# Kernel optimization log

Hardware: AMD Instinct MI355X
Metric: run time of the kernel (lower is better)

The kernel has to match this reference:

```python
import jax, jax.numpy as jnp
import numpy as np

N, D_IN, R, D_OUT, U = 500000, 128, 256, 64, 10000
EPS = 1e-8


def _vb_layer(m, v, W_mu, W_lv, relu_out):
    # Variational Bayes linear layer, moment propagation:
    #   out_mean = m @ W_mu
    #   out_var  = v @ (W_mu^2 + W_var) + m^2 @ W_var,  W_var = exp(W_lv)
    W_var = jnp.exp(W_lv)
    M = m @ W_mu
    V = v @ (W_mu * W_mu + W_var) + (m * m) @ W_var
    if relu_out:
        gate = (M > 0).astype(M.dtype)
        M = M * gate
        V = V * gate
    return M, V


def setup_inputs() -> dict:
    key = jax.random.key(0)
    ks = jax.random.split(key, 6)
    X = jax.random.normal(ks[0], (N, D_IN), jnp.float32)
    X_idx = jnp.sort(jax.random.randint(ks[1], (N,), 0, U, dtype=jnp.int32))
    W_mu0 = jax.random.normal(ks[2], (D_IN, R), jnp.float32) / np.sqrt(D_IN)
    W_lv0 = jax.random.normal(ks[3], (D_IN, R), jnp.float32) * 0.1 - 4.0
    W_mu1 = jax.random.normal(ks[4], (R, D_OUT), jnp.float32) / np.sqrt(R)
    W_lv1 = jax.random.normal(ks[5], (R, D_OUT), jnp.float32) * 0.1 - 4.0
    return {"X": X, "X_idx": X_idx, "W_mu0": W_mu0, "W_lv0": W_lv0,
            "W_mu1": W_mu1, "W_lv1": W_lv1}


def reference(X, X_idx, W_mu0, W_lv0, W_mu1, W_lv1):
    m, v = _vb_layer(X, jnp.zeros_like(X), W_mu0, W_lv0, True)   # [N, R]
    m, v = _vb_layer(m, v, W_mu1, W_lv1, False)                  # [N, D_OUT]
    v = jnp.maximum(v, EPS)
    inv_v = 1.0 / v
    # precision-weighted aggregation per group id (replaces per-uid loop)
    var_inv_sum = jax.ops.segment_sum(inv_v, X_idx, num_segments=U) + EPS
    mean_sum = jax.ops.segment_sum(m * inv_v, X_idx, num_segments=U)
    emb_var = 1.0 / var_inv_sum          # [U, D_OUT]
    emb_mean = mean_sum * emb_var        # [U, D_OUT]
    return emb_mean, emb_var
```

## Files before the change

kernel.cpp:

```cpp
#include <hip/hip_runtime.h>
#include <stdint.h>

#define N_ROWS 500000
#define U_DIM 10000
#define EPSV 1e-8f
#define NT16 31250

typedef __attribute__((ext_vector_type(8))) short bf16x8;
typedef __attribute__((ext_vector_type(4))) float f32x4;

__device__ __forceinline__ short f2bf(float f) {
  unsigned u = __float_as_uint(f);
  u += 0x7fffu + ((u >> 16) & 1u);
  return (short)(u >> 16);
}
__device__ __forceinline__ float bf2f(short s) {
  return __uint_as_float(((unsigned)(unsigned short)s) << 16);
}

__global__ void prep_weights(const float* __restrict__ Wmu0,
                             const float* __restrict__ Wlv0,
                             const float* __restrict__ Wmu1,
                             const float* __restrict__ Wlv1,
                             short* __restrict__ wgt) {
  int i = blockIdx.x * blockDim.x + threadIdx.x;
  if (i < 32768) {
    int c = i & 255, k = i >> 8;
    int rc = c >> 5, ct = (c >> 4) & 1, n = c & 15;
    int kt = k >> 5, q = (k >> 3) & 3, u = k & 7;
    int lane = q * 16 + n;
    float mu = Wmu0[k * 256 + c];
    float ev = __expf(Wlv0[k * 256 + c]);
    wgt[((((rc * 2 + 0) * 2 + ct) * 4 + kt) * 64 + lane) * 8 + u] = f2bf(mu);
    wgt[((((rc * 2 + 1) * 2 + ct) * 4 + kt) * 64 + lane) * 8 + u] = f2bf(ev);
  } else if (i < 49152) {
    int i2 = i - 32768;
    int o = i2 & 63, j = i2 >> 6;
    int rc = j >> 5, q = (j >> 3) & 3, u = j & 7;
    int ct1 = o >> 4, n = o & 15;
    int lane = q * 16 + n;
    float mu = Wmu1[j * 64 + o];
    float ev = __expf(Wlv1[j * 64 + o]);
    int b = 65536 + (((rc * 4 + ct1) * 3 + 0) * 64 + lane) * 8 + u;
    wgt[b]        = f2bf(mu);
    wgt[b + 512]  = f2bf(mu * mu + ev);
    wgt[b + 1024] = f2bf(ev);
  }
}

__global__ __launch_bounds__(256, 3) void vb_fused(
    const float* __restrict__ X, const int* __restrict__ Xidx,
    const short* __restrict__ wgt, float* __restrict__ out) {
  __shared__ __align__(16) short stage[2][8192];
  __shared__ __align__(16) short ldsM[4][16 * 40];
  __shared__ __align__(16) short ldsV[4][16 * 40];

  const int tid  = threadIdx.x;
  const int w    = tid >> 6;
  const int lane = tid & 63;
  const int n    = lane & 15;
  const int q    = lane >> 4;
  const int T    = blockIdx.x * 4 + w;
  const bool active = (T < NT16);
  const int row0 = active ? T * 16 : (N_ROWS - 16);

  const f32x4 zf4 = {0.f, 0.f, 0.f, 0.f};
  const int lane8 = lane * 8;

  bf16x8 a_m[4], a_sq[4];
  {
    const float* xr = X + (size_t)(row0 + n) * 128;
#pragma unroll
    for (int kt = 0; kt < 4; ++kt) {
      float xf[8];
      *(float4*)&xf[0] = *(const float4*)&xr[kt * 32 + q * 8];
      *(float4*)&xf[4] = *(const float4*)&xr[kt * 32 + q * 8 + 4];
#pragma unroll
      for (int u = 0; u < 8; ++u) {
        a_m[kt][u]  = f2bf(xf[u]);
        a_sq[kt][u] = f2bf(xf[u] * xf[u]);
      }
    }
  }

  f32x4 accm1[4], accv1[4];
#pragma unroll
  for (int c = 0; c < 4; ++c) { accm1[c] = zf4; accv1[c] = zf4; }

  const char* gbase = (const char*)wgt;
#define ISSUE_STAGE(rc_, buf_)                                                 \
  do {                                                                         \
    _Pragma("unroll")                                                          \
    for (int s_ = 0; s_ < 4; ++s_) {                                           \
      __builtin_amdgcn_global_load_lds(                                        \
          (const __attribute__((address_space(1))) unsigned int*)              \
              (gbase + (rc_) * 16384 + s_ * 4096 + tid * 16),                  \
          (__attribute__((address_space(3))) unsigned int*)                    \
              ((char*)&stage[buf_][0] + s_ * 4096 + (w << 10)),                \
          16, 0, 0);                                                           \
    }                                                                          \
  } while (0)

  ISSUE_STAGE(0, 0);

#pragma unroll
  for (int rc = 0; rc < 8; ++rc) {
    __syncthreads();
    if (rc < 7) ISSUE_STAGE(rc + 1, (rc + 1) & 1);

    const short* st = &stage[rc & 1][0];

    f32x4 accm0[2], accv0[2];
    accm0[0] = zf4; accm0[1] = zf4; accv0[0] = zf4; accv0[1] = zf4;
#pragma unroll
    for (int kt = 0; kt < 4; ++kt) {
#pragma unroll
      for (int ct = 0; ct < 2; ++ct) {
        bf16x8 bm = *(const bf16x8*)&st[((0 * 2 + ct) * 4 + kt) * 512 + lane8];
        bf16x8 bv = *(const bf16x8*)&st[((1 * 2 + ct) * 4 + kt) * 512 + lane8];
        accm0[ct] = __builtin_amdgcn_mfma_f32_16x16x32_bf16(a_m[kt],  bm, accm0[ct], 0, 0, 0);
        accv0[ct] = __builtin_amdgcn_mfma_f32_16x16x32_bf16(a_sq[kt], bv, accv0[ct], 0, 0, 0);
      }
    }

#pragma unroll
    for (int ct = 0; ct < 2; ++ct) {
      const int c = ct * 16 + n;
#pragma unroll
      for (int reg = 0; reg < 4; ++reg) {
        float m = accm0[ct][reg], v = accv0[ct][reg];
        if (!(m > 0.f)) { m = 0.f; v = 0.f; }
        const int row = q * 4 + reg;
        ldsM[w][row * 40 + c] = f2bf(m);
        ldsV[w][row * 40 + c] = f2bf(v);
      }
    }
    bf16x8 am = *(const bf16x8*)&ldsM[w][n * 40 + q * 8];
    bf16x8 av = *(const bf16x8*)&ldsV[w][n * 40 + q * 8];
    bf16x8 asq;
#pragma unroll
    for (int u = 0; u < 8; ++u) {
      float f = bf2f(am[u]);
      asq[u] = f2bf(f * f);
    }

    const short* l1b = wgt + 65536 + rc * 6144 + lane8;
#pragma unroll
    for (int ct1 = 0; ct1 < 4; ++ct1) {
      const short* fb = l1b + ct1 * 1536;
      bf16x8 b1 = *(const bf16x8*)&fb[0];
      bf16x8 b2 = *(const bf16x8*)&fb[512];
      bf16x8 b3 = *(const bf16x8*)&fb[1024];
      accm1[ct1] = __builtin_amdgcn_mfma_f32_16x16x32_bf16(am,  b1, accm1[ct1], 0, 0, 0);
      accv1[ct1] = __builtin_amdgcn_mfma_f32_16x16x32_bf16(av,  b2, accv1[ct1], 0, 0, 0);
      accv1[ct1] = __builtin_amdgcn_mfma_f32_16x16x32_bf16(asq, b3, accv1[ct1], 0, 0, 0);
    }
  }
#undef ISSUE_STAGE

  if (!active) return;
  float* meanp = out;
  float* varp  = out + U_DIM * 64;
  int4 idx4 = *(const int4*)&Xidx[row0 + q * 4];
  int uid[4] = {idx4.x, idx4.y, idx4.z, idx4.w};
#pragma unroll
  for (int ct = 0; ct < 4; ++ct) {
    const int o = ct * 16 + n;
    float sm = 0.f, sv = 0.f;
    int cur = uid[0];
#pragma unroll
    for (int reg = 0; reg < 4; ++reg) {
      float v1 = fmaxf(accv1[ct][reg], EPSV);
      float inv = 1.0f / v1;
      float mi  = accm1[ct][reg] * inv;
      if (uid[reg] != cur) {
        atomicAdd(&meanp[cur * 64 + o], sm);
        atomicAdd(&varp[cur * 64 + o], sv);
        sm = 0.f; sv = 0.f; cur = uid[reg];
      }
      sm += mi; sv += inv;
    }
    atomicAdd(&meanp[cur * 64 + o], sm);
    atomicAdd(&varp[cur * 64 + o], sv);
  }
}

__global__ void finalize(float* __restrict__ out) {
  int i = blockIdx.x * blockDim.x + threadIdx.x;
  if (i < U_DIM * 64) {
    float s = out[U_DIM * 64 + i];
    float var = 1.0f / (s + EPSV);
    out[U_DIM * 64 + i] = var;
    out[i] = out[i] * var;
  }
}

extern "C" void kernel_launch(void* const* d_in, const int* in_sizes, int n_in,
                              void* d_out, int out_size, void* d_ws, size_t ws_size,
                              hipStream_t stream) {
  (void)in_sizes; (void)n_in; (void)out_size; (void)ws_size;
  const float* X    = (const float*)d_in[0];
  const int*   Xidx = (const int*)d_in[1];
  const float* Wmu0 = (const float*)d_in[2];
  const float* Wlv0 = (const float*)d_in[3];
  const float* Wmu1 = (const float*)d_in[4];
  const float* Wlv1 = (const float*)d_in[5];
  float* out = (float*)d_out;
  short* wgt = (short*)d_ws;

  hipMemsetAsync(d_out, 0, (size_t)U_DIM * 64 * 2 * sizeof(float), stream);
  prep_weights<<<192, 256, 0, stream>>>(Wmu0, Wlv0, Wmu1, Wlv1, wgt);
  vb_fused<<<7813, 256, 0, stream>>>(X, Xidx, wgt, out);
  finalize<<<(U_DIM * 64 + 255) / 256, 256, 0, stream>>>(out);
}
```

Measured before the change: 555.9 us.

## Make fused VB kernel persistent with full layer-0 weights resident in LDS

Switches from one-tile-per-wave blocks to a persistent grid of 256 blocks of 8 waves. Each block loads all 128 KB of layer-0 weights into LDS once, then loops over 16-row tiles with a stride of 2048. Each wave prefetches the next tile's X rows into registers while computing the current one. This removes the per-block restaging of weights and the per-stage barriers, at the cost of lower occupancy from the large LDS footprint. With 256 blocks on 256 CUs there is only one block per CU.

```diff
diff --git a/kernel.cpp b/kernel.cpp
--- a/kernel.cpp
+++ b/kernel.cpp
@@ -48,140 +48,158 @@
   }
 }
 
-__global__ __launch_bounds__(256, 3) void vb_fused(
+__global__ __launch_bounds__(512, 2) void vb_fused(
     const float* __restrict__ X, const int* __restrict__ Xidx,
     const short* __restrict__ wgt, float* __restrict__ out) {
-  __shared__ __align__(16) short stage[2][8192];
-  __shared__ __align__(16) short ldsM[4][16 * 40];
-  __shared__ __align__(16) short ldsV[4][16 * 40];
+  __shared__ __align__(16) short stage[65536];
+  __shared__ __align__(16) short ldsM[8][16 * 40];
+  __shared__ __align__(16) short ldsV[8][16 * 40];
 
   const int tid  = threadIdx.x;
   const int w    = tid >> 6;
   const int lane = tid & 63;
   const int n    = lane & 15;
   const int q    = lane >> 4;
-  const int T    = blockIdx.x * 4 + w;
-  const bool active = (T < NT16);
-  const int row0 = active ? T * 16 : (N_ROWS - 16);
-
+  const int lane8 = lane * 8;
+
+  {
+    const char* gbase = (const char*)wgt;
+#pragma unroll
+    for (int s = 0; s < 16; ++s) {
+      __builtin_amdgcn_global_load_lds(
+          (const __attribute__((address_space(1))) unsigned int*)
+              (gbase + s * 8192 + tid * 16),
+          (__attribute__((address_space(3))) unsigned int*)
+              ((char*)&stage[0] + s * 8192 + (w << 10)),
+          16, 0, 0);
+    }
+  }
+  __syncthreads();
+
+  const int gw = blockIdx.x * 8 + w;
+  int T = gw;
+
+  float* meanp = out;
+  float* varp  = out + U_DIM * 64;
   const f32x4 zf4 = {0.f, 0.f, 0.f, 0.f};
-  const int lane8 = lane * 8;
-
-  bf16x8 a_m[4], a_sq[4];
+
+  float4 xr[8];
   {
-    const float* xr = X + (size_t)(row0 + n) * 128;
+    const float* xp = X + (size_t)(T * 16 + n) * 128 + q * 8;
+#pragma unroll
+    for (int kt = 0; kt < 4; ++kt) {
+      xr[kt * 2]     = *(const float4*)(xp + kt * 32);
+      xr[kt * 2 + 1] = *(const float4*)(xp + kt * 32 + 4);
+    }
+  }
+
+  while (true) {
+    bf16x8 a_m[4], a_sq[4];
 #pragma unroll
     for (int kt = 0; kt < 4; ++kt) {
       float xf[8];
-      *(float4*)&xf[0] = *(const float4*)&xr[kt * 32 + q * 8];
-      *(float4*)&xf[4] = *(const float4*)&xr[kt * 32 + q * 8 + 4];
+      *(float4*)&xf[0] = xr[kt * 2];
+      *(float4*)&xf[4] = xr[kt * 2 + 1];
 #pragma unroll
       for (int u = 0; u < 8; ++u) {
         a_m[kt][u]  = f2bf(xf[u]);
         a_sq[kt][u] = f2bf(xf[u] * xf[u]);
       }
     }
-  }
-
-  f32x4 accm1[4], accv1[4];
-#pragma unroll
-  for (int c = 0; c < 4; ++c) { accm1[c] = zf4; accv1[c] = zf4; }
-
-  const char* gbase = (const char*)wgt;
-#define ISSUE_STAGE(rc_, buf_)                                                 \
-  do {                                                                         \
-    _Pragma("unroll")                                                          \
-    for (int s_ = 0; s_ < 4; ++s_) {                                           \
-      __builtin_amdgcn_global_load_lds(                                        \
-          (const __attribute__((address_space(1))) unsigned int*)              \
-              (gbase + (rc_) * 16384 + s_ * 4096 + tid * 16),                  \
-          (__attribute__((address_space(3))) unsigned int*)                    \
-              ((char*)&stage[buf_][0] + s_ * 4096 + (w << 10)),                \
-          16, 0, 0);                                                           \
-    }                                                                          \
-  } while (0)
-
-  ISSUE_STAGE(0, 0);
-
-#pragma unroll
-  for (int rc = 0; rc < 8; ++rc) {
-    __syncthreads();
-    if (rc < 7) ISSUE_STAGE(rc + 1, (rc + 1) & 1);
-
-    const short* st = &stage[rc & 1][0];
-
-    f32x4 accm0[2], accv0[2];
-    accm0[0] = zf4; accm0[1] = zf4; accv0[0] = zf4; accv0[1] = zf4;
-#pragma unroll
-    for (int kt = 0; kt < 4; ++kt) {
+
+    const int Tcur = T;
+    const int Tn   = T + 2048;
+    if (Tn < NT16) {
+      const float* xp = X + (size_t)(Tn * 16 + n) * 128 + q * 8;
+#pragma unroll
+      for (int kt = 0; kt < 4; ++kt) {
+        xr[kt * 2]     = *(const float4*)(xp + kt * 32);
+        xr[kt * 2 + 1] = *(const float4*)(xp + kt * 32 + 4);
+      }
+    }
+
+    f32x4 accm1[4], accv1[4];
+#pragma unroll
+    for (int c = 0; c < 4; ++c) { accm1[c] = zf4; accv1[c] = zf4; }
+
+#pragma unroll
+    for (int rc = 0; rc < 8; ++rc) {
+      const short* st = &stage[rc * 8192];
+
+      f32x4 accm0[2], accv0[2];
+      accm0[0] = zf4; accm0[1] = zf4; accv0[0] = zf4; accv0[1] = zf4;
+#pragma unroll
+      for (int kt = 0; kt < 4; ++kt) {
+#pragma unroll
+        for (int ct = 0; ct < 2; ++ct) {
+          bf16x8 bm = *(const bf16x8*)&st[((0 * 2 + ct) * 4 + kt) * 512 + lane8];
+          bf16x8 bv = *(const bf16x8*)&st[((1 * 2 + ct) * 4 + kt) * 512 + lane8];
+          accm0[ct] = __builtin_amdgcn_mfma_f32_16x16x32_bf16(a_m[kt],  bm, accm0[ct], 0, 0, 0);
+          accv0[ct] = __builtin_amdgcn_mfma_f32_16x16x32_bf16(a_sq[kt], bv, accv0[ct], 0, 0, 0);
+        }
+      }
+
 #pragma unroll
       for (int ct = 0; ct < 2; ++ct) {
-        bf16x8 bm = *(const bf16x8*)&st[((0 * 2 + ct) * 4 + kt) * 512 + lane8];
-        bf16x8 bv = *(const bf16x8*)&st[((1 * 2 + ct) * 4 + kt) * 512 + lane8];
-        accm0[ct] = __builtin_amdgcn_mfma_f32_16x16x32_bf16(a_m[kt],  bm, accm0[ct], 0, 0, 0);
-        accv0[ct] = __builtin_amdgcn_mfma_f32_16x16x32_bf16(a_sq[kt], bv, accv0[ct], 0, 0, 0);
-      }
-    }
-
-#pragma unroll
-    for (int ct = 0; ct < 2; ++ct) {
-      const int c = ct * 16 + n;
-#pragma unroll
-      for (int reg = 0; reg < 4; ++reg) {
-        float m = accm0[ct][reg], v = accv0[ct][reg];
-        if (!(m > 0.f)) { m = 0.f; v = 0.f; }
-        const int row = q * 4 + reg;
-        ldsM[w][row * 40 + c] = f2bf(m);
-        ldsV[w][row * 40 + c] = f2bf(v);
-      }
-    }
-    bf16x8 am = *(const bf16x8*)&ldsM[w][n * 40 + q * 8];
-    bf16x8 av = *(const bf16x8*)&ldsV[w][n * 40 + q * 8];
-    bf16x8 asq;
-#pragma unroll
-    for (int u = 0; u < 8; ++u) {
-      float f = bf2f(am[u]);
-      asq[u] = f2bf(f * f);
-    }
-
-    const short* l1b = wgt + 65536 + rc * 6144 + lane8;
-#pragma unroll
-    for (int ct1 = 0; ct1 < 4; ++ct1) {
-      const short* fb = l1b + ct1 * 1536;
-      bf16x8 b1 = *(const bf16x8*)&fb[0];
-      bf16x8 b2 = *(const bf16x8*)&fb[512];
-      bf16x8 b3 = *(const bf16x8*)&fb[1024];
-      accm1[ct1] = __builtin_amdgcn_mfma_f32_16x16x32_bf16(am,  b1, accm1[ct1], 0, 0, 0);
-      accv1[ct1] = __builtin_amdgcn_mfma_f32_16x16x32_bf16(av,  b2, accv1[ct1], 0, 0, 0);
-      accv1[ct1] = __builtin_amdgcn_mfma_f32_16x16x32_bf16(asq, b3, accv1[ct1], 0, 0, 0);
-    }
-  }
-#undef ISSUE_STAGE
-
-  if (!active) return;
-  float* meanp = out;
-  float* varp  = out + U_DIM * 64;
-  int4 idx4 = *(const int4*)&Xidx[row0 + q * 4];
-  int uid[4] = {idx4.x, idx4.y, idx4.z, idx4.w};
-#pragma unroll
-  for (int ct = 0; ct < 4; ++ct) {
-    const int o = ct * 16 + n;
-    float sm = 0.f, sv = 0.f;
-    int cur = uid[0];
-#pragma unroll
-    for (int reg = 0; reg < 4; ++reg) {
-      float v1 = fmaxf(accv1[ct][reg], EPSV);
-      float inv = 1.0f / v1;
-      float mi  = accm1[ct][reg] * inv;
-      if (uid[reg] != cur) {
+        const int c = ct * 16 + n;
+#pragma unroll
+        for (int reg = 0; reg < 4; ++reg) {
+          float m = accm0[ct][reg], v = accv0[ct][reg];
+          if (!(m > 0.f)) { m = 0.f; v = 0.f; }
+          const int row = q * 4 + reg;
+          ldsM[w][row * 40 + c] = f2bf(m);
+          ldsV[w][row * 40 + c] = f2bf(v);
+        }
+      }
+      bf16x8 am = *(const bf16x8*)&ldsM[w][n * 40 + q * 8];
+      bf16x8 av = *(const bf16x8*)&ldsV[w][n * 40 + q * 8];
+      bf16x8 asq;
+#pragma unroll
+      for (int u = 0; u < 8; ++u) {
+        float f = bf2f(am[u]);
+        asq[u] = f2bf(f * f);
+      }
+
+      const short* l1b = wgt + 65536 + rc * 6144 + lane8;
+#pragma unroll
+      for (int ct1 = 0; ct1 < 4; ++ct1) {
+        const short* fb = l1b + ct1 * 1536;
+        bf16x8 b1 = *(const bf16x8*)&fb[0];
+        bf16x8 b2 = *(const bf16x8*)&fb[512];
+        bf16x8 b3 = *(const bf16x8*)&fb[1024];
+        accm1[ct1] = __builtin_amdgcn_mfma_f32_16x16x32_bf16(am,  b1, accm1[ct1], 0, 0, 0);
+        accv1[ct1] = __builtin_amdgcn_mfma_f32_16x16x32_bf16(av,  b2, accv1[ct1], 0, 0, 0);
+        accv1[ct1] = __builtin_amdgcn_mfma_f32_16x16x32_bf16(asq, b3, accv1[ct1], 0, 0, 0);
+      }
+    }
+
+    {
+      int4 idx4 = *(const int4*)&Xidx[Tcur * 16 + q * 4];
+      int uid[4] = {idx4.x, idx4.y, idx4.z, idx4.w};
+#pragma unroll
+      for (int ct = 0; ct < 4; ++ct) {
+        const int o = ct * 16 + n;
+        float sm = 0.f, sv = 0.f;
+        int cur = uid[0];
+#pragma unroll
+        for (int reg = 0; reg < 4; ++reg) {
+          float v1 = fmaxf(accv1[ct][reg], EPSV);
+          float inv = 1.0f / v1;
+          float mi  = accm1[ct][reg] * inv;
+          if (uid[reg] != cur) {
+            atomicAdd(&meanp[cur * 64 + o], sm);
+            atomicAdd(&varp[cur * 64 + o], sv);
+            sm = 0.f; sv = 0.f; cur = uid[reg];
+          }
+          sm += mi; sv += inv;
+        }
         atomicAdd(&meanp[cur * 64 + o], sm);
         atomicAdd(&varp[cur * 64 + o], sv);
-        sm = 0.f; sv = 0.f; cur = uid[reg];
-      }
-      sm += mi; sv += inv;
-    }
-    atomicAdd(&meanp[cur * 64 + o], sm);
-    atomicAdd(&varp[cur * 64 + o], sv);
+      }
+    }
+
+    if (Tn >= NT16) break;
+    T = Tn;
   }
 }
 
@@ -210,6 +228,6 @@
 
   hipMemsetAsync(d_out, 0, (size_t)U_DIM * 64 * 2 * sizeof(float), stream);
   prep_weights<<<192, 256, 0, stream>>>(Wmu0, Wlv0, Wmu1, Wlv1, wgt);
-  vb_fused<<<7813, 256, 0, stream>>>(X, Xidx, wgt, out);
+  vb_fused<<<256, 512, 0, stream>>>(X, Xidx, wgt, out);
   finalize<<<(U_DIM * 64 + 255) / 256, 256, 0, stream>>>(out);
 }
```

Result: slower. 870.7 us (+56.6%).

## Process two 16-row tiles per wave to reuse staged weights

Applied to the files above, without the earlier changes.

Each wave now handles 32 rows as two 16-row MFMA tiles, sharing every weight fragment loaded from LDS and global across both tiles. The grid is halved accordingly, and the LDS scratch for layer-0 activations is doubled. This cuts the weight staging, barrier and fragment-load overhead per row. The cost is higher register pressure under the existing launch bounds, with possible spills, and fewer blocks in flight.

```diff
diff --git a/kernel.cpp b/kernel.cpp
--- a/kernel.cpp
+++ b/kernel.cpp
@@ -4,7 +4,7 @@
 #define N_ROWS 500000
 #define U_DIM 10000
 #define EPSV 1e-8f
-#define NT16 31250
+#define NT32 15625
 
 typedef __attribute__((ext_vector_type(8))) short bf16x8;
 typedef __attribute__((ext_vector_type(4))) float f32x4;
@@ -52,8 +52,8 @@
     const float* __restrict__ X, const int* __restrict__ Xidx,
     const short* __restrict__ wgt, float* __restrict__ out) {
   __shared__ __align__(16) short stage[2][8192];
-  __shared__ __align__(16) short ldsM[4][16 * 40];
-  __shared__ __align__(16) short ldsV[4][16 * 40];
+  __shared__ __align__(16) short ldsM[4][2][16 * 40];
+  __shared__ __align__(16) short ldsV[4][2][16 * 40];
 
   const int tid  = threadIdx.x;
   const int w    = tid >> 6;
@@ -61,15 +61,16 @@
   const int n    = lane & 15;
   const int q    = lane >> 4;
   const int T    = blockIdx.x * 4 + w;
-  const bool active = (T < NT16);
-  const int row0 = active ? T * 16 : (N_ROWS - 16);
+  const bool active = (T < NT32);
+  const int row0 = active ? T * 32 : (N_ROWS - 32);
 
   const f32x4 zf4 = {0.f, 0.f, 0.f, 0.f};
   const int lane8 = lane * 8;
 
-  bf16x8 a_m[4], a_sq[4];
-  {
-    const float* xr = X + (size_t)(row0 + n) * 128;
+  bf16x8 a_m[2][4], a_sq[2][4];
+#pragma unroll
+  for (int t = 0; t < 2; ++t) {
+    const float* xr = X + (size_t)(row0 + t * 16 + n) * 128;
 #pragma unroll
     for (int kt = 0; kt < 4; ++kt) {
       float xf[8];
@@ -77,15 +78,17 @@
       *(float4*)&xf[4] = *(const float4*)&xr[kt * 32 + q * 8 + 4];
 #pragma unroll
       for (int u = 0; u < 8; ++u) {
-        a_m[kt][u]  = f2bf(xf[u]);
-        a_sq[kt][u] = f2bf(xf[u] * xf[u]);
-      }
-    }
-  }
-
-  f32x4 accm1[4], accv1[4];
-#pragma unroll
-  for (int c = 0; c < 4; ++c) { accm1[c] = zf4; accv1[c] = zf4; }
+        a_m[t][kt][u]  = f2bf(xf[u]);
+        a_sq[t][kt][u] = f2bf(xf[u] * xf[u]);
+      }
+    }
+  }
+
+  f32x4 accm1[2][4], accv1[2][4];
+#pragma unroll
+  for (int t = 0; t < 2; ++t)
+#pragma unroll
+    for (int c = 0; c < 4; ++c) { accm1[t][c] = zf4; accv1[t][c] = zf4; }
 
   const char* gbase = (const char*)wgt;
 #define ISSUE_STAGE(rc_, buf_)                                                 \
@@ -110,38 +113,43 @@
 
     const short* st = &stage[rc & 1][0];
 
-    f32x4 accm0[2], accv0[2];
-    accm0[0] = zf4; accm0[1] = zf4; accv0[0] = zf4; accv0[1] = zf4;
-#pragma unroll
-    for (int kt = 0; kt < 4; ++kt) {
-#pragma unroll
-      for (int ct = 0; ct < 2; ++ct) {
+#pragma unroll
+    for (int ct = 0; ct < 2; ++ct) {
+      f32x4 am0_0 = zf4, am0_1 = zf4, av0_0 = zf4, av0_1 = zf4;
+#pragma unroll
+      for (int kt = 0; kt < 4; ++kt) {
         bf16x8 bm = *(const bf16x8*)&st[((0 * 2 + ct) * 4 + kt) * 512 + lane8];
         bf16x8 bv = *(const bf16x8*)&st[((1 * 2 + ct) * 4 + kt) * 512 + lane8];
-        accm0[ct] = __builtin_amdgcn_mfma_f32_16x16x32_bf16(a_m[kt],  bm, accm0[ct], 0, 0, 0);
-        accv0[ct] = __builtin_amdgcn_mfma_f32_16x16x32_bf16(a_sq[kt], bv, accv0[ct], 0, 0, 0);
-      }
-    }
-
-#pragma unroll
-    for (int ct = 0; ct < 2; ++ct) {
+        am0_0 = __builtin_amdgcn_mfma_f32_16x16x32_bf16(a_m[0][kt],  bm, am0_0, 0, 0, 0);
+        am0_1 = __builtin_amdgcn_mfma_f32_16x16x32_bf16(a_m[1][kt],  bm, am0_1, 0, 0, 0);
+        av0_0 = __builtin_amdgcn_mfma_f32_16x16x32_bf16(a_sq[0][kt], bv, av0_0, 0, 0, 0);
+        av0_1 = __builtin_amdgcn_mfma_f32_16x16x32_bf16(a_sq[1][kt], bv, av0_1, 0, 0, 0);
+      }
       const int c = ct * 16 + n;
 #pragma unroll
       for (int reg = 0; reg < 4; ++reg) {
-        float m = accm0[ct][reg], v = accv0[ct][reg];
-        if (!(m > 0.f)) { m = 0.f; v = 0.f; }
         const int row = q * 4 + reg;
-        ldsM[w][row * 40 + c] = f2bf(m);
-        ldsV[w][row * 40 + c] = f2bf(v);
-      }
-    }
-    bf16x8 am = *(const bf16x8*)&ldsM[w][n * 40 + q * 8];
-    bf16x8 av = *(const bf16x8*)&ldsV[w][n * 40 + q * 8];
-    bf16x8 asq;
-#pragma unroll
-    for (int u = 0; u < 8; ++u) {
-      float f = bf2f(am[u]);
-      asq[u] = f2bf(f * f);
+        float m0 = am0_0[reg], v0 = av0_0[reg];
+        if (!(m0 > 0.f)) { m0 = 0.f; v0 = 0.f; }
+        ldsM[w][0][row * 40 + c] = f2bf(m0);
+        ldsV[w][0][row * 40 + c] = f2bf(v0);
+        float m1 = am0_1[reg], v1 = av0_1[reg];
+        if (!(m1 > 0.f)) { m1 = 0.f; v1 = 0.f; }
+        ldsM[w][1][row * 40 + c] = f2bf(m1);
+        ldsV[w][1][row * 40 + c] = f2bf(v1);
+      }
+    }
+
+    bf16x8 am[2], av[2], asq[2];
+#pragma unroll
+    for (int t = 0; t < 2; ++t) {
+      am[t] = *(const bf16x8*)&ldsM[w][t][n * 40 + q * 8];
+      av[t] = *(const bf16x8*)&ldsV[w][t][n * 40 + q * 8];
+#pragma unroll
+      for (int u = 0; u < 8; ++u) {
+        float f = bf2f(am[t][u]);
+        asq[t][u] = f2bf(f * f);
+      }
     }
 
     const short* l1b = wgt + 65536 + rc * 6144 + lane8;
@@ -151,9 +159,12 @@
       bf16x8 b1 = *(const bf16x8*)&fb[0];
       bf16x8 b2 = *(const bf16x8*)&fb[512];
       bf16x8 b3 = *(const bf16x8*)&fb[1024];
-      accm1[ct1] = __builtin_amdgcn_mfma_f32_16x16x32_bf16(am,  b1, accm1[ct1], 0, 0, 0);
-      accv1[ct1] = __builtin_amdgcn_mfma_f32_16x16x32_bf16(av,  b2, accv1[ct1], 0, 0, 0);
-      accv1[ct1] = __builtin_amdgcn_mfma_f32_16x16x32_bf16(asq, b3, accv1[ct1], 0, 0, 0);
+#pragma unroll
+      for (int t = 0; t < 2; ++t) {
+        accm1[t][ct1] = __builtin_amdgcn_mfma_f32_16x16x32_bf16(am[t],  b1, accm1[t][ct1], 0, 0, 0);
+        accv1[t][ct1] = __builtin_amdgcn_mfma_f32_16x16x32_bf16(av[t],  b2, accv1[t][ct1], 0, 0, 0);
+        accv1[t][ct1] = __builtin_amdgcn_mfma_f32_16x16x32_bf16(asq[t], b3, accv1[t][ct1], 0, 0, 0);
+      }
     }
   }
 #undef ISSUE_STAGE
@@ -161,27 +172,30 @@
   if (!active) return;
   float* meanp = out;
   float* varp  = out + U_DIM * 64;
-  int4 idx4 = *(const int4*)&Xidx[row0 + q * 4];
-  int uid[4] = {idx4.x, idx4.y, idx4.z, idx4.w};
-#pragma unroll
-  for (int ct = 0; ct < 4; ++ct) {
-    const int o = ct * 16 + n;
-    float sm = 0.f, sv = 0.f;
-    int cur = uid[0];
-#pragma unroll
-    for (int reg = 0; reg < 4; ++reg) {
-      float v1 = fmaxf(accv1[ct][reg], EPSV);
-      float inv = 1.0f / v1;
-      float mi  = accm1[ct][reg] * inv;
-      if (uid[reg] != cur) {
-        atomicAdd(&meanp[cur * 64 + o], sm);
-        atomicAdd(&varp[cur * 64 + o], sv);
-        sm = 0.f; sv = 0.f; cur = uid[reg];
-      }
-      sm += mi; sv += inv;
-    }
-    atomicAdd(&meanp[cur * 64 + o], sm);
-    atomicAdd(&varp[cur * 64 + o], sv);
+#pragma unroll
+  for (int t = 0; t < 2; ++t) {
+    int4 idx4 = *(const int4*)&Xidx[row0 + t * 16 + q * 4];
+    int uid[4] = {idx4.x, idx4.y, idx4.z, idx4.w};
+#pragma unroll
+    for (int ct = 0; ct < 4; ++ct) {
+      const int o = ct * 16 + n;
+      float sm = 0.f, sv = 0.f;
+      int cur = uid[0];
+#pragma unroll
+      for (int reg = 0; reg < 4; ++reg) {
+        float v1 = fmaxf(accv1[t][ct][reg], EPSV);
+        float inv = 1.0f / v1;
+        float mi  = accm1[t][ct][reg] * inv;
+        if (uid[reg] != cur) {
+          atomicAdd(&meanp[cur * 64 + o], sm);
+          atomicAdd(&varp[cur * 64 + o], sv);
+          sm = 0.f; sv = 0.f; cur = uid[reg];
+        }
+        sm += mi; sv += inv;
+      }
+      atomicAdd(&meanp[cur * 64 + o], sm);
+      atomicAdd(&varp[cur * 64 + o], sv);
+    }
   }
 }
 
@@ -210,6 +224,6 @@
 
   hipMemsetAsync(d_out, 0, (size_t)U_DIM * 64 * 2 * sizeof(float), stream);
   prep_weights<<<192, 256, 0, stream>>>(Wmu0, Wlv0, Wmu1, Wlv1, wgt);
-  vb_fused<<<7813, 256, 0, stream>>>(X, Xidx, wgt, out);
+  vb_fused<<<3907, 256, 0, stream>>>(X, Xidx, wgt, out);
   finalize<<<(U_DIM * 64 + 255) / 256, 256, 0, stream>>>(out);
 }
```

After: 735.9 us. 32.4% more time.
